# Optimization experiments

Hardware: AMD Instinct MI355X
Metric: run time of the kernel (lower is better)

Reference implementation:

```python
import jax, jax.numpy as jnp
import numpy as np

N_NODES = 100000
N_EDGES = 1600000
NUM_GRAPHS = 128


def setup_inputs() -> dict:
    key = jax.random.key(0)
    k1, k2, k3, k4, k5, k6 = jax.random.split(key, 6)
    x = jax.random.normal(k1, (N_NODES, 69), dtype=jnp.float32)
    src = jax.random.randint(k2, (N_EDGES,), 0, N_NODES)
    dst = jax.random.randint(k3, (N_EDGES,), 0, N_NODES)
    graph_ids = jnp.sort(jax.random.randint(k4, (N_NODES,), 0, NUM_GRAPHS))
    # Glorot-uniform weights like dgl GraphConv (bias=False)
    lim1 = np.sqrt(6.0 / (69 + 128))
    lim2 = np.sqrt(6.0 / (128 + 64))
    W1 = jax.random.uniform(k5, (69, 128), minval=-lim1, maxval=lim1, dtype=jnp.float32)
    W2 = jax.random.uniform(k6, (128, 64), minval=-lim2, maxval=lim2, dtype=jnp.float32)
    return {"x": x, "W1": W1, "W2": W2, "src": src, "dst": dst, "graph_ids": graph_ids}


def _graph_conv(feat, W, src, dst, inv_sqrt_out, inv_sqrt_in, n_nodes):
    # dgl GraphConv norm='both': D_out^{-1/2} -> SpMM(A) -> D_in^{-1/2} -> W
    h = feat * inv_sqrt_out[:, None]
    agg = jax.ops.segment_sum(h[src], dst, num_segments=n_nodes)  # [N, d]
    agg = agg * inv_sqrt_in[:, None]
    return agg @ W


def reference(x, W1, W2, src, dst, graph_ids):
    n = x.shape[0]
    ones = jnp.ones((src.shape[0],), dtype=x.dtype)
    out_deg = jax.ops.segment_sum(ones, src, num_segments=n)
    in_deg = jax.ops.segment_sum(ones, dst, num_segments=n)
    inv_sqrt_out = jax.lax.rsqrt(jnp.clip(out_deg, 1.0, None))
    inv_sqrt_in = jax.lax.rsqrt(jnp.clip(in_deg, 1.0, None))

    h = _graph_conv(x, W1, src, dst, inv_sqrt_out, inv_sqrt_in, n)
    h = jax.nn.relu(h)
    h = _graph_conv(h, W2, src, dst, inv_sqrt_out, inv_sqrt_in, n)
    h = jax.nn.relu(h)
    # dgl.max_nodes: per-graph max readout -> [num_graphs, 64]
    readout = jax.ops.segment_max(h, graph_ids, num_segments=NUM_GRAPHS)
    return readout
```

## Files before the change

kernel.cpp:

```cpp
#include <hip/hip_runtime.h>

#define N_NODES 100000
#define N_EDGES 1600000
#define NUM_GRAPHS 128

#define BSH 10
#define NBUCK 98
#define NBLKP 500
#define EPB (N_EDGES / NBLKP)
#define SOFF (NBUCK * NBLKP)
#define NSCAN (2 * NBUCK * NBLKP)
#define SCAN_BS 1024
#define NBSC ((NSCAN + SCAN_BS - 1) / SCAN_BS)

__device__ __forceinline__ unsigned bf16pair(float a, float b) {
    unsigned ua = __float_as_uint(a), ub = __float_as_uint(b);
    ua = (ua + 0x7FFFu + ((ua >> 16) & 1u)) >> 16;
    ub = (ub + 0x7FFFu + ((ub >> 16) & 1u)) >> 16;
    return ua | (ub << 16);
}
__device__ __forceinline__ float bflo(unsigned u) { return __uint_as_float(u << 16); }
__device__ __forceinline__ float bfhi(unsigned u) { return __uint_as_float(u & 0xFFFF0000u); }

__global__ __launch_bounds__(256) void part_hist(const int* __restrict__ src,
                                                 const int* __restrict__ dst,
                                                 int* __restrict__ cnt) {
    __shared__ int hd[4 * NBUCK], hs[4 * NBUCK];
    int t = threadIdx.x;
    for (int i = t; i < 4 * NBUCK; i += 256) { hd[i] = 0; hs[i] = 0; }
    __syncthreads();
    int wid = t >> 6;
    int* hdw = hd + wid * NBUCK;
    int* hsw = hs + wid * NBUCK;
    int e0 = blockIdx.x * EPB;
    for (int j = 4 * t; j + 3 < EPB; j += 1024) {
        int4 s4 = *(const int4*)(src + e0 + j);
        int4 d4 = *(const int4*)(dst + e0 + j);
        atomicAdd(&hdw[d4.x >> BSH], 1); atomicAdd(&hdw[d4.y >> BSH], 1);
        atomicAdd(&hdw[d4.z >> BSH], 1); atomicAdd(&hdw[d4.w >> BSH], 1);
        atomicAdd(&hsw[s4.x >> BSH], 1); atomicAdd(&hsw[s4.y >> BSH], 1);
        atomicAdd(&hsw[s4.z >> BSH], 1); atomicAdd(&hsw[s4.w >> BSH], 1);
    }
    __syncthreads();
    int bk = blockIdx.x;
    for (int i = t; i < NBUCK; i += 256) {
        cnt[i * NBLKP + bk] = hd[i] + hd[NBUCK + i] + hd[2 * NBUCK + i] + hd[3 * NBUCK + i];
        cnt[SOFF + i * NBLKP + bk] = hs[i] + hs[NBUCK + i] + hs[2 * NBUCK + i] + hs[3 * NBUCK + i];
    }
}

__global__ __launch_bounds__(256) void scan1(const int* __restrict__ cnt, int* __restrict__ excl,
                                             int* __restrict__ blksum, int n) {
    __shared__ int tmp[256];
    int t = threadIdx.x;
    int idx0 = blockIdx.x * SCAN_BS + t * 4;
    int v[4];
#pragma unroll
    for (int k = 0; k < 4; ++k) { int i = idx0 + k; v[k] = (i < n) ? cnt[i] : 0; }
    int sum = v[0] + v[1] + v[2] + v[3];
    tmp[t] = sum;
    __syncthreads();
    for (int off = 1; off < 256; off <<= 1) {
        int y = (t >= off) ? tmp[t - off] : 0;
        __syncthreads();
        tmp[t] += y;
        __syncthreads();
    }
    int run = (t > 0) ? tmp[t - 1] : 0;
#pragma unroll
    for (int k = 0; k < 4; ++k) { int i = idx0 + k; if (i < n) excl[i] = run; run += v[k]; }
    if (t == 255) blksum[blockIdx.x] = tmp[255];
}

__global__ __launch_bounds__(256) void scan2(int* __restrict__ blksum, int nb) {
    __shared__ int tmp[256];
    int t = threadIdx.x;
    int C = (nb + 255) / 256;
    int base = t * C;
    int s = 0;
    for (int k = 0; k < C; ++k) { int i = base + k; if (i < nb) s += blksum[i]; }
    tmp[t] = s;
    __syncthreads();
    for (int off = 1; off < 256; off <<= 1) {
        int y = (t >= off) ? tmp[t - off] : 0;
        __syncthreads();
        tmp[t] += y;
        __syncthreads();
    }
    int run = (t > 0) ? tmp[t - 1] : 0;
    for (int k = 0; k < C; ++k) {
        int i = base + k;
        if (i < nb) { int v = blksum[i]; blksum[i] = run; run += v; }
    }
}

__global__ __launch_bounds__(256) void part_scatter(const int* __restrict__ src,
                                                    const int* __restrict__ dst,
                                                    const int* __restrict__ cnt,
                                                    const int* __restrict__ blk,
                                                    unsigned* __restrict__ pdst,
                                                    unsigned short* __restrict__ psrc) {
    __shared__ int cd[NBUCK], cs[NBUCK];
    int bk = blockIdx.x;
    int t = threadIdx.x;
    for (int i = t; i < NBUCK; i += 256) {
        int ii = i * NBLKP + bk;
        cd[i] = cnt[ii] + blk[ii >> 10];
        int jj = SOFF + i * NBLKP + bk;
        cs[i] = cnt[jj] + blk[jj >> 10] - N_EDGES;
    }
    __syncthreads();
    int e0 = bk * EPB;
    for (int j = 4 * t; j + 3 < EPB; j += 1024) {
        int4 s4 = *(const int4*)(src + e0 + j);
        int4 d4 = *(const int4*)(dst + e0 + j);
        int ss[4] = { s4.x, s4.y, s4.z, s4.w };
        int dd[4] = { d4.x, d4.y, d4.z, d4.w };
#pragma unroll
        for (int u = 0; u < 4; ++u) {
            int s = ss[u], d = dd[u];
            int pd = atomicAdd(&cd[d >> BSH], 1);
            pdst[pd] = (unsigned)s | ((unsigned)(d & 1023) << 17);
            int ps = atomicAdd(&cs[s >> BSH], 1);
            psrc[ps] = (unsigned short)(s & 1023);
        }
    }
}

__global__ __launch_bounds__(1024) void phase_d(const unsigned* __restrict__ pdst,
                                                const unsigned short* __restrict__ psrc,
                                                const int* __restrict__ cnt,
                                                const int* __restrict__ blk,
                                                int* __restrict__ ecol, int* __restrict__ row_start,
                                                float* __restrict__ isqi, float* __restrict__ isqo,
                                                int nN) {
    __shared__ int lh[1024];
    __shared__ int lsc[1024];
    int t = threadIdx.x;
    if (blockIdx.x < NBUCK) {
        int bu = blockIdx.x;
        int i0 = bu * NBLKP;
        int b0 = cnt[i0] + blk[i0 >> 10];
        int b1;
        if (bu == NBUCK - 1) b1 = N_EDGES;
        else { int i1 = i0 + NBLKP; b1 = cnt[i1] + blk[i1 >> 10]; }
        lh[t] = 0;
        __syncthreads();
        for (int j = b0 + t; j < b1; j += 1024)
            atomicAdd(&lh[pdst[j] >> 17], 1);
        __syncthreads();
        int myc = lh[t];
        lsc[t] = myc;
        __syncthreads();
        for (int off = 1; off < 1024; off <<= 1) {
            int y = (t >= off) ? lsc[t - off] : 0;
            __syncthreads();
            lsc[t] += y;
            __syncthreads();
        }
        int excl = lsc[t] - myc;
        int node = (bu << BSH) + t;
        if (node < nN) {
            row_start[node] = b0 + excl;
            isqi[node] = rsqrtf(fmaxf((float)myc, 1.0f));
        }
        __syncthreads();
        lh[t] = b0 + excl;
        __syncthreads();
        for (int j = b0 + t; j < b1; j += 1024) {
            unsigned w = pdst[j];
            int pos = atomicAdd(&lh[w >> 17], 1);
            ecol[pos] = (int)(w & 0x1FFFFu);
        }
    } else {
        int bu = blockIdx.x - NBUCK;
        int i0 = SOFF + bu * NBLKP;
        int b0 = cnt[i0] + blk[i0 >> 10] - N_EDGES;
        int b1;
        if (bu == NBUCK - 1) b1 = N_EDGES;
        else { int i1 = i0 + NBLKP; b1 = cnt[i1] + blk[i1 >> 10] - N_EDGES; }
        lh[t] = 0;
        __syncthreads();
        for (int j = b0 + t; j < b1; j += 1024)
            atomicAdd(&lh[psrc[j]], 1);
        __syncthreads();
        int node = (bu << BSH) + t;
        if (node < nN) isqo[node] = rsqrtf(fmaxf((float)lh[t], 1.0f));
    }
}

__global__ void prescale_kernel(const float* __restrict__ x, const float* __restrict__ isqo,
                                unsigned* __restrict__ xmain, unsigned* __restrict__ xtail, int nN) {
    int wave = (int)(((unsigned)blockIdx.x * blockDim.x + threadIdx.x) >> 6);
    int lane = threadIdx.x & 63;
    if (wave >= nN || lane >= 36) return;
    float s = isqo[wave];
    int c = 2 * lane;
    float a = (c < 69) ? x[(size_t)wave * 69 + c] * s : 0.0f;
    float b = (c + 1 < 69) ? x[(size_t)wave * 69 + c + 1] * s : 0.0f;
    unsigned p = bf16pair(a, b);
    if (lane < 32) xmain[(size_t)wave * 32 + lane] = p;
    else           xtail[(size_t)wave * 4 + (lane - 32)] = p;
}

__global__ void gather1_kernel(const unsigned* __restrict__ xmain, const unsigned* __restrict__ xtail,
                               const int* __restrict__ ecol, const int* __restrict__ row_start,
                               const float* __restrict__ dscale, float* __restrict__ agg,
                               int nN, int nE) {
    int wave = (int)(((unsigned)blockIdx.x * blockDim.x + threadIdx.x) >> 6);
    int lane = threadIdx.x & 63;
    if (wave >= nN) return;
    int beg = row_start[wave];
    int end = (wave == nN - 1) ? nE : row_start[wave + 1];
    int half = lane >> 5;
    int c = lane & 31;
    bool tact = (c < 4);
    float ax = 0.0f, ay = 0.0f, tx = 0.0f, ty = 0.0f;
    for (int j0 = beg; j0 < end; j0 += 64) {
        int ne = min(64, end - j0);
        int eidx = (lane < ne) ? ecol[j0 + lane] : 0;
        int k = 0;
        for (; k + 16 <= ne; k += 16) {
            unsigned v[8], tv[8];
#pragma unroll
            for (int u = 0; u < 8; ++u) {
                int s = __shfl(eidx, k + 2 * u + half);
                v[u] = xmain[(size_t)s * 32 + c];
                tv[u] = tact ? xtail[(size_t)s * 4 + c] : 0u;
            }
#pragma unroll
            for (int u = 0; u < 8; ++u) {
                ax += bflo(v[u]); ay += bfhi(v[u]);
                tx += bflo(tv[u]); ty += bfhi(tv[u]);
            }
        }
        for (; k + 2 <= ne; k += 2) {
            int s = __shfl(eidx, k + half);
            unsigned v = xmain[(size_t)s * 32 + c];
            ax += bflo(v); ay += bfhi(v);
            if (tact) { unsigned tv = xtail[(size_t)s * 4 + c]; tx += bflo(tv); ty += bfhi(tv); }
        }
        if (k < ne) {
            int s = __shfl(eidx, k);
            if (half == 0) {
                unsigned v = xmain[(size_t)s * 32 + c];
                ax += bflo(v); ay += bfhi(v);
                if (tact) { unsigned tv = xtail[(size_t)s * 4 + c]; tx += bflo(tv); ty += bfhi(tv); }
            }
        }
    }
    ax += __shfl_xor(ax, 32); ay += __shfl_xor(ay, 32);
    tx += __shfl_xor(tx, 32); ty += __shfl_xor(ty, 32);
    if (half == 0) {
        float dsc = dscale[wave];
        ((float2*)(agg + (size_t)wave * 72))[c] = make_float2(ax * dsc, ay * dsc);
        if (tact)
            ((float2*)(agg + (size_t)wave * 72 + 64))[c] = make_float2(tx * dsc, ty * dsc);
    }
}

__global__ void gather2_kernel(const unsigned* __restrict__ feat, const int* __restrict__ ecol,
                               const int* __restrict__ row_start, const float* __restrict__ dscale,
                               float* __restrict__ agg, int nN, int nE) {
    int wave = (int)(((unsigned)blockIdx.x * blockDim.x + threadIdx.x) >> 6);
    int lane = threadIdx.x & 63;
    if (wave >= nN) return;
    int beg = row_start[wave];
    int end = (wave == nN - 1) ? nE : row_start[wave + 1];
    int half = lane >> 5;
    int c = lane & 31;
    float ax = 0.0f, ay = 0.0f;
    for (int j0 = beg; j0 < end; j0 += 64) {
        int ne = min(64, end - j0);
        int eidx = (lane < ne) ? ecol[j0 + lane] : 0;
        int k = 0;
        for (; k + 16 <= ne; k += 16) {
            unsigned v[8];
#pragma unroll
            for (int u = 0; u < 8; ++u) {
                int s = __shfl(eidx, k + 2 * u + half);
                v[u] = feat[(size_t)s * 32 + c];
            }
#pragma unroll
            for (int u = 0; u < 8; ++u) { ax += bflo(v[u]); ay += bfhi(v[u]); }
        }
        for (; k + 2 <= ne; k += 2) {
            int s = __shfl(eidx, k + half);
            unsigned v = feat[(size_t)s * 32 + c];
            ax += bflo(v); ay += bfhi(v);
        }
        if (k < ne) {
            int s = __shfl(eidx, k);
            if (half == 0) {
                unsigned v = feat[(size_t)s * 32 + c];
                ax += bflo(v); ay += bfhi(v);
            }
        }
    }
    ax += __shfl_xor(ax, 32);
    ay += __shfl_xor(ay, 32);
    if (half == 0) {
        float dsc = dscale[wave];
        ((float2*)(agg + (size_t)wave * 64))[c] = make_float2(ax * dsc, ay * dsc);
    }
}

template<int KP, int K, int NO, bool RELU, bool SCALE, bool BF16OUT, bool BF16IN>
__global__ __launch_bounds__(256) void node_gemm(const void* __restrict__ in,
                                                 const float* __restrict__ W,
                                                 const float* __restrict__ rowscale,
                                                 void* __restrict__ out, int nN) {
    constexpr int CG = NO / 8;
    constexpr int RT = 256 / CG;
    constexpr int ROWS = RT * 4;
    __shared__ float Wl[KP * NO];
    for (int i = threadIdx.x; i < KP * NO; i += 256)
        Wl[i] = (i < K * NO) ? W[i] : 0.0f;
    __syncthreads();

    int cg = threadIdx.x % CG;
    int rt = threadIdx.x / CG;
    int row0 = blockIdx.x * ROWS + rt * 4;
    int c0 = cg * 8;

    float4 accL[4] = {};
    float4 accH[4] = {};
    int rclamp[4];
#pragma unroll
    for (int r = 0; r < 4; ++r) rclamp[r] = min(row0 + r, nN - 1);

    if (BF16IN) {
        const unsigned* inu = (const unsigned*)in;
#pragma unroll 2
        for (int k8 = 0; k8 < KP / 8; ++k8) {
            uint4 a4[4];
#pragma unroll
            for (int r = 0; r < 4; ++r)
                a4[r] = *(const uint4*)(inu + (size_t)rclamp[r] * (KP / 2) + k8 * 4);
#pragma unroll
            for (int kk = 0; kk < 8; ++kk) {
                int k = k8 * 8 + kk;
                float4 wlo = *(const float4*)&Wl[k * NO + c0];
                float4 whi = *(const float4*)&Wl[k * NO + c0 + 4];
#pragma unroll
                for (int r = 0; r < 4; ++r) {
                    unsigned wd = ((const unsigned*)&a4[r])[kk >> 1];
                    float ar = (kk & 1) ? bfhi(wd) : bflo(wd);
                    accL[r].x += ar * wlo.x; accL[r].y += ar * wlo.y;
                    accL[r].z += ar * wlo.z; accL[r].w += ar * wlo.w;
                    accH[r].x += ar * whi.x; accH[r].y += ar * whi.y;
                    accH[r].z += ar * whi.z; accH[r].w += ar * whi.w;
                }
            }
        }
    } else {
        const float* inf = (const float*)in;
#pragma unroll 2
        for (int k4 = 0; k4 < KP / 4; ++k4) {
            float4 a[4];
#pragma unroll
            for (int r = 0; r < 4; ++r)
                a[r] = *(const float4*)(inf + (size_t)rclamp[r] * KP + k4 * 4);
#pragma unroll
            for (int kk = 0; kk < 4; ++kk) {
                int k = k4 * 4 + kk;
                float4 wlo = *(const float4*)&Wl[k * NO + c0];
                float4 whi = *(const float4*)&Wl[k * NO + c0 + 4];
#pragma unroll
                for (int r = 0; r < 4; ++r) {
                    float ar = (kk == 0) ? a[r].x : (kk == 1) ? a[r].y : (kk == 2) ? a[r].z : a[r].w;
                    accL[r].x += ar * wlo.x; accL[r].y += ar * wlo.y;
                    accL[r].z += ar * wlo.z; accL[r].w += ar * wlo.w;
                    accH[r].x += ar * whi.x; accH[r].y += ar * whi.y;
                    accH[r].z += ar * whi.z; accH[r].w += ar * whi.w;
                }
            }
        }
    }

#pragma unroll
    for (int r = 0; r < 4; ++r) {
        int row = row0 + r;
        if (row < nN) {
            float4 lo = accL[r], hi = accH[r];
            if (SCALE) {
                float sc = rowscale[row];
                lo.x *= sc; lo.y *= sc; lo.z *= sc; lo.w *= sc;
                hi.x *= sc; hi.y *= sc; hi.z *= sc; hi.w *= sc;
            }
            if (RELU) {
                lo.x = fmaxf(lo.x, 0.f); lo.y = fmaxf(lo.y, 0.f);
                lo.z = fmaxf(lo.z, 0.f); lo.w = fmaxf(lo.w, 0.f);
                hi.x = fmaxf(hi.x, 0.f); hi.y = fmaxf(hi.y, 0.f);
                hi.z = fmaxf(hi.z, 0.f); hi.w = fmaxf(hi.w, 0.f);
            }
            if (BF16OUT) {
                unsigned* ob = (unsigned*)out;
                uint4 p;
                p.x = bf16pair(lo.x, lo.y); p.y = bf16pair(lo.z, lo.w);
                p.z = bf16pair(hi.x, hi.y); p.w = bf16pair(hi.z, hi.w);
                *(uint4*)(ob + (size_t)row * (NO / 2) + c0 / 2) = p;
            } else {
                float* of = (float*)out;
                *(float4*)(of + (size_t)row * NO + c0) = lo;
                *(float4*)(of + (size_t)row * NO + c0 + 4) = hi;
            }
        }
    }
}

__global__ void readout_kernel(const float* __restrict__ agg2, const int* __restrict__ gid,
                               unsigned* __restrict__ out, int nN) {
    const int NPW = 32;
    int wave = (int)(((unsigned)blockIdx.x * blockDim.x + threadIdx.x) >> 6);
    int lane = threadIdx.x & 63;
    int n0 = wave * NPW;
    if (n0 >= nN) return;
    int curg = gid[n0];
    float best = 0.0f;
    for (int i = 0; i < NPW; ++i) {
        int n = n0 + i;
        if (n >= nN) break;
        int g = gid[n];
        float v = fmaxf(agg2[(size_t)n * 64 + lane], 0.0f);
        if (g != curg) {
            atomicMax(&out[curg * 64 + lane], __float_as_uint(best));
            curg = g;
            best = v;
        } else {
            best = fmaxf(best, v);
        }
    }
    atomicMax(&out[curg * 64 + lane], __float_as_uint(best));
}

extern "C" void kernel_launch(void* const* d_in, const int* in_sizes, int n_in,
                              void* d_out, int out_size, void* d_ws, size_t ws_size,
                              hipStream_t stream) {
    const float* x   = (const float*)d_in[0];
    const float* W1  = (const float*)d_in[1];
    const float* W2  = (const float*)d_in[2];
    const int*   src = (const int*)d_in[3];
    const int*   dst = (const int*)d_in[4];
    const int*   gid = (const int*)d_in[5];

    char* w = (char*)d_ws;
    float* isqo    = (float*)w;                 w += N_NODES * 4;
    float* isqi    = (float*)w;                 w += N_NODES * 4;
    int* row_start = (int*)w;                   w += N_NODES * 4;
    int* ecol      = (int*)w;                   w += (size_t)N_EDGES * 4;
    int* cnt       = (int*)w;                   w += (size_t)NSCAN * 4;
    int* blksum    = (int*)w;                   w += 1024 * 4;
    float* bufA    = (float*)w;                 w += (size_t)N_NODES * 72 * 4;
    char* bufB     = w;
    unsigned* pdst       = (unsigned*)bufB;
    unsigned* xmain      = (unsigned*)bufB;
    unsigned* xtail      = (unsigned*)(bufB + (size_t)N_NODES * 32 * 4);
    unsigned short* psrc = (unsigned short*)(bufB + (size_t)N_NODES * 36 * 4);
    unsigned* h1         = (unsigned*)bufB;
    float* agg2          = (float*)bufB;

    hipMemsetAsync(d_out, 0, (size_t)out_size * sizeof(float), stream);

    part_hist<<<NBLKP, 256, 0, stream>>>(src, dst, cnt);
    scan1<<<NBSC, 256, 0, stream>>>(cnt, cnt, blksum, NSCAN);
    scan2<<<1, 256, 0, stream>>>(blksum, NBSC);
    part_scatter<<<NBLKP, 256, 0, stream>>>(src, dst, cnt, blksum, pdst, psrc);
    phase_d<<<2 * NBUCK, 1024, 0, stream>>>(pdst, psrc, cnt, blksum, ecol, row_start,
                                            isqi, isqo, N_NODES);
    prescale_kernel<<<(N_NODES * 64 + 255) / 256, 256, 0, stream>>>(x, isqo, xmain, xtail, N_NODES);

    gather1_kernel<<<(N_NODES * 64 + 255) / 256, 256, 0, stream>>>(
        xmain, xtail, ecol, row_start, isqi, bufA, N_NODES, N_EDGES);
    node_gemm<72, 69, 128, true, false, true, false><<<(N_NODES + 63) / 64, 256, 0, stream>>>(
        (const void*)bufA, W1, nullptr, (void*)h1, N_NODES);

    node_gemm<128, 128, 64, false, true, true, true><<<(N_NODES + 127) / 128, 256, 0, stream>>>(
        (const void*)h1, W2, isqo, (void*)bufA, N_NODES);
    gather2_kernel<<<(N_NODES * 64 + 255) / 256, 256, 0, stream>>>(
        (const unsigned*)bufA, ecol, row_start, isqi, agg2, N_NODES, N_EDGES);

    readout_kernel<<<((N_NODES + 31) / 32 * 64 + 255) / 256, 256, 0, stream>>>(
        agg2, gid, (unsigned*)d_out, N_NODES);
}
```

Measured before the change: 277.6 us.

## Fuse layer-1 gather with W1 GEMM and ReLU in one kernel

Merges the first-layer sparse gather and the dense W1 multiply into a single kernel. Each wave aggregates one node's 72-wide bf16 row, then multiplies it by W1 held in LDS via shuffles, applies ReLU and writes bf16 h1 directly. The prescaled input is also packed into one 36-word-per-node array instead of separate main and tail arrays. This drops the fp32 aggregation buffer round trip and one launch. The cost is 1024-thread blocks with 36 KB of LDS each, which may limit occupancy, a per-wave scalar GEMM instead of a tiled one, and gathers that now use only 36 of 64 lanes.

```diff
diff --git a/kernel.cpp b/kernel.cpp
--- a/kernel.cpp
+++ b/kernel.cpp
@@ -190,7 +190,7 @@
 }
 
 __global__ void prescale_kernel(const float* __restrict__ x, const float* __restrict__ isqo,
-                                unsigned* __restrict__ xmain, unsigned* __restrict__ xtail, int nN) {
+                                unsigned* __restrict__ xsu, int nN) {
     int wave = (int)(((unsigned)blockIdx.x * blockDim.x + threadIdx.x) >> 6);
     int lane = threadIdx.x & 63;
     if (wave >= nN || lane >= 36) return;
@@ -198,65 +198,71 @@
     int c = 2 * lane;
     float a = (c < 69) ? x[(size_t)wave * 69 + c] * s : 0.0f;
     float b = (c + 1 < 69) ? x[(size_t)wave * 69 + c + 1] * s : 0.0f;
-    unsigned p = bf16pair(a, b);
-    if (lane < 32) xmain[(size_t)wave * 32 + lane] = p;
-    else           xtail[(size_t)wave * 4 + (lane - 32)] = p;
-}
-
-__global__ void gather1_kernel(const unsigned* __restrict__ xmain, const unsigned* __restrict__ xtail,
-                               const int* __restrict__ ecol, const int* __restrict__ row_start,
-                               const float* __restrict__ dscale, float* __restrict__ agg,
-                               int nN, int nE) {
-    int wave = (int)(((unsigned)blockIdx.x * blockDim.x + threadIdx.x) >> 6);
+    xsu[(size_t)wave * 36 + lane] = bf16pair(a, b);
+}
+
+__global__ __launch_bounds__(1024) void gather1_gemm1(const unsigned* __restrict__ xsu,
+                                                      const int* __restrict__ ecol,
+                                                      const int* __restrict__ row_start,
+                                                      const float* __restrict__ dscale,
+                                                      const float* __restrict__ W1,
+                                                      unsigned* __restrict__ h1, int nN, int nE) {
+    __shared__ float Wl[72 * 128];
+    for (int i = threadIdx.x; i < 72 * 128; i += 1024)
+        Wl[i] = (i < 69 * 128) ? W1[i] : 0.0f;
+    __syncthreads();
+
+    int wave = blockIdx.x * 16 + (threadIdx.x >> 6);
     int lane = threadIdx.x & 63;
     if (wave >= nN) return;
     int beg = row_start[wave];
     int end = (wave == nN - 1) ? nE : row_start[wave + 1];
-    int half = lane >> 5;
-    int c = lane & 31;
-    bool tact = (c < 4);
-    float ax = 0.0f, ay = 0.0f, tx = 0.0f, ty = 0.0f;
+    bool act = (lane < 36);
+    float ax = 0.0f, ay = 0.0f;
     for (int j0 = beg; j0 < end; j0 += 64) {
         int ne = min(64, end - j0);
         int eidx = (lane < ne) ? ecol[j0 + lane] : 0;
         int k = 0;
-        for (; k + 16 <= ne; k += 16) {
-            unsigned v[8], tv[8];
+        for (; k + 8 <= ne; k += 8) {
+            unsigned v[8];
 #pragma unroll
             for (int u = 0; u < 8; ++u) {
-                int s = __shfl(eidx, k + 2 * u + half);
-                v[u] = xmain[(size_t)s * 32 + c];
-                tv[u] = tact ? xtail[(size_t)s * 4 + c] : 0u;
-            }
-#pragma unroll
-            for (int u = 0; u < 8; ++u) {
-                ax += bflo(v[u]); ay += bfhi(v[u]);
-                tx += bflo(tv[u]); ty += bfhi(tv[u]);
-            }
+                int s = __shfl(eidx, k + u);
+                v[u] = act ? xsu[(size_t)s * 36 + lane] : 0u;
+            }
+#pragma unroll
+            for (int u = 0; u < 8; ++u) { ax += bflo(v[u]); ay += bfhi(v[u]); }
         }
         for (; k + 2 <= ne; k += 2) {
-            int s = __shfl(eidx, k + half);
-            unsigned v = xmain[(size_t)s * 32 + c];
+            int s0 = __shfl(eidx, k), s1 = __shfl(eidx, k + 1);
+            unsigned v0 = act ? xsu[(size_t)s0 * 36 + lane] : 0u;
+            unsigned v1 = act ? xsu[(size_t)s1 * 36 + lane] : 0u;
+            ax += bflo(v0) + bflo(v1); ay += bfhi(v0) + bfhi(v1);
+        }
+        for (; k < ne; ++k) {
+            int s = __shfl(eidx, k);
+            unsigned v = act ? xsu[(size_t)s * 36 + lane] : 0u;
             ax += bflo(v); ay += bfhi(v);
-            if (tact) { unsigned tv = xtail[(size_t)s * 4 + c]; tx += bflo(tv); ty += bfhi(tv); }
-        }
-        if (k < ne) {
-            int s = __shfl(eidx, k);
-            if (half == 0) {
-                unsigned v = xmain[(size_t)s * 32 + c];
-                ax += bflo(v); ay += bfhi(v);
-                if (tact) { unsigned tv = xtail[(size_t)s * 4 + c]; tx += bflo(tv); ty += bfhi(tv); }
-            }
-        }
-    }
-    ax += __shfl_xor(ax, 32); ay += __shfl_xor(ay, 32);
-    tx += __shfl_xor(tx, 32); ty += __shfl_xor(ty, 32);
-    if (half == 0) {
-        float dsc = dscale[wave];
-        ((float2*)(agg + (size_t)wave * 72))[c] = make_float2(ax * dsc, ay * dsc);
-        if (tact)
-            ((float2*)(agg + (size_t)wave * 72 + 64))[c] = make_float2(tx * dsc, ty * dsc);
-    }
+        }
+    }
+    float dsc = dscale[wave];
+    float a0 = act ? ax * dsc : 0.0f;
+    float a1 = act ? ay * dsc : 0.0f;
+
+    float acc0 = 0.0f, acc1 = 0.0f;
+    int c2 = 2 * lane;
+#pragma unroll 4
+    for (int kk = 0; kk < 36; ++kk) {
+        float v0 = __shfl(a0, kk);
+        float v1 = __shfl(a1, kk);
+        float2 w0 = *(const float2*)&Wl[(2 * kk) * 128 + c2];
+        float2 w1 = *(const float2*)&Wl[(2 * kk + 1) * 128 + c2];
+        acc0 += v0 * w0.x + v1 * w1.x;
+        acc1 += v0 * w0.y + v1 * w1.y;
+    }
+    acc0 = fmaxf(acc0, 0.0f);
+    acc1 = fmaxf(acc1, 0.0f);
+    h1[(size_t)wave * 64 + lane] = bf16pair(acc0, acc1);
 }
 
 __global__ void gather2_kernel(const unsigned* __restrict__ feat, const int* __restrict__ ecol,
@@ -451,14 +457,14 @@
     int* ecol      = (int*)w;                   w += (size_t)N_EDGES * 4;
     int* cnt       = (int*)w;                   w += (size_t)NSCAN * 4;
     int* blksum    = (int*)w;                   w += 1024 * 4;
-    float* bufA    = (float*)w;                 w += (size_t)N_NODES * 72 * 4;
+    char* bufA     = w;                         w += (size_t)N_NODES * 72 * 4;
     char* bufB     = w;
     unsigned* pdst       = (unsigned*)bufB;
-    unsigned* xmain      = (unsigned*)bufB;
-    unsigned* xtail      = (unsigned*)(bufB + (size_t)N_NODES * 32 * 4);
+    unsigned* xsu        = (unsigned*)bufB;
     unsigned short* psrc = (unsigned short*)(bufB + (size_t)N_NODES * 36 * 4);
-    unsigned* h1         = (unsigned*)bufB;
-    float* agg2          = (float*)bufB;
+    unsigned* h1         = (unsigned*)bufA;
+    unsigned* y2s        = (unsigned*)bufB;
+    float* agg2          = (float*)bufA;
 
     hipMemsetAsync(d_out, 0, (size_t)out_size * sizeof(float), stream);
 
@@ -468,17 +474,15 @@
     part_scatter<<<NBLKP, 256, 0, stream>>>(src, dst, cnt, blksum, pdst, psrc);
     phase_d<<<2 * NBUCK, 1024, 0, stream>>>(pdst, psrc, cnt, blksum, ecol, row_start,
                                             isqi, isqo, N_NODES);
-    prescale_kernel<<<(N_NODES * 64 + 255) / 256, 256, 0, stream>>>(x, isqo, xmain, xtail, N_NODES);
-
-    gather1_kernel<<<(N_NODES * 64 + 255) / 256, 256, 0, stream>>>(
-        xmain, xtail, ecol, row_start, isqi, bufA, N_NODES, N_EDGES);
-    node_gemm<72, 69, 128, true, false, true, false><<<(N_NODES + 63) / 64, 256, 0, stream>>>(
-        (const void*)bufA, W1, nullptr, (void*)h1, N_NODES);
+    prescale_kernel<<<(N_NODES * 64 + 255) / 256, 256, 0, stream>>>(x, isqo, xsu, N_NODES);
+
+    gather1_gemm1<<<(N_NODES + 15) / 16, 1024, 0, stream>>>(
+        xsu, ecol, row_start, isqi, W1, h1, N_NODES, N_EDGES);
 
     node_gemm<128, 128, 64, false, true, true, true><<<(N_NODES + 127) / 128, 256, 0, stream>>>(
-        (const void*)h1, W2, isqo, (void*)bufA, N_NODES);
+        (const void*)h1, W2, isqo, (void*)y2s, N_NODES);
     gather2_kernel<<<(N_NODES * 64 + 255) / 256, 256, 0, stream>>>(
-        (const unsigned*)bufA, ecol, row_start, isqi, agg2, N_NODES, N_EDGES);
+        y2s, ecol, row_start, isqi, agg2, N_NODES, N_EDGES);
 
     readout_kernel<<<((N_NODES + 31) / 32 * 64 + 255) / 256, 256, 0, stream>>>(
         agg2, gid, (unsigned*)d_out, N_NODES);
```

New measurement: 353.1 us. 27.2% more time.
